# Kernel optimization log

Hardware: AMD Instinct MI355X
Metric: run time of the kernel (lower is better)

The kernel has to match this reference:

```python
import jax, jax.numpy as jnp
import numpy as np

D_MODEL = 512
N_HEADS = 8
D_FF = 2048
EPS = 1e-5


def _layernorm(x, g, b):
    mu = jnp.mean(x, axis=-1, keepdims=True)
    var = jnp.mean(jnp.square(x - mu), axis=-1, keepdims=True)
    return (x - mu) * jax.lax.rsqrt(var + EPS) * g + b


def setup_inputs() -> dict:
    key = jax.random.key(0)
    ks = jax.random.split(key, 12)
    B, N, C = 2, 2048, D_MODEL
    s = lambda fi, fo: 1.0 / np.sqrt(fi)
    inp = {
        "x": jax.random.normal(ks[0], (B, N, C), jnp.float32),
        # weights stored as [in, out] (y = x @ W + b)
        "qkv_w": jax.random.normal(ks[1], (C, 3 * C), jnp.float32) * s(C, 3 * C),
        "qkv_b": jnp.zeros((3 * C,), jnp.float32),
        "out_w": jax.random.normal(ks[2], (C, C), jnp.float32) * s(C, C),
        "out_b": jnp.zeros((C,), jnp.float32),
        "ffn_w1": jax.random.normal(ks[3], (C, D_FF), jnp.float32) * s(C, D_FF),
        "ffn_b1": jnp.zeros((D_FF,), jnp.float32),
        "ffn_w2": jax.random.normal(ks[4], (D_FF, C), jnp.float32) * s(D_FF, C),
        "ffn_b2": jnp.zeros((C,), jnp.float32),
        "n1_g": jnp.ones((C,), jnp.float32),
        "n1_b": jnp.zeros((C,), jnp.float32),
        "n2_g": jnp.ones((C,), jnp.float32),
        "n2_b": jnp.zeros((C,), jnp.float32),
        "conv_w": jax.random.normal(ks[5], (C, C, 3), jnp.float32) * s(3 * C, C),  # [out, in, k]
        "conv_b": jnp.zeros((C,), jnp.float32),
        "cn_g": jnp.ones((C,), jnp.float32),
        "cn_b": jnp.zeros((C,), jnp.float32),
    }
    return inp


def _forward(x, qkv_w, qkv_b, out_w, out_b, ffn_w1, ffn_b1, ffn_w2, ffn_b2,
             n1_g, n1_b, n2_g, n2_b, conv_w, conv_b, cn_g, cn_b):
    B, N, C = x.shape
    H, dk = N_HEADS, C // N_HEADS
    scale = 1.0 / np.sqrt(dk)

    # --- ProbSparse self-attention ---
    qkv = (x @ qkv_w + qkv_b).reshape(B, N, 3, H, dk)
    q, k, v = (jnp.moveaxis(qkv, (2, 3), (0, 2))[i] for i in range(3))  # each [B,H,N,dk]
    scores = jnp.einsum("bhnd,bhmd->bhnm", q, k) * scale  # [B,H,N,N]
    M = jnp.max(scores, axis=-1) - jnp.mean(scores, axis=-1)  # [B,H,N]
    n_top = max(1, min(int(N * 0.25), N - 1))
    _, top_idx = jax.lax.top_k(M, n_top)  # [B,H,n_top]
    bidx = jnp.arange(B)[:, None, None]
    hidx = jnp.arange(H)[None, :, None]
    row_sel = jnp.zeros((B, H, N), bool).at[bidx, hidx, top_idx].set(True)
    # rows not selected are fully masked (-1e9) -> uniform softmax, as in the original
    attn = jax.nn.softmax(jnp.where(row_sel[..., None], scores, -1e9), axis=-1)
    out = jnp.einsum("bhnm,bhmd->bhnd", attn, v)
    out = out.transpose(0, 2, 1, 3).reshape(B, N, C)
    attn_out = out @ out_w + out_b

    x = _layernorm(x + attn_out, n1_g, n1_b)

    # --- FFN (exact GELU) ---
    h = jax.nn.gelu(x @ ffn_w1 + ffn_b1, approximate=False)
    ffn_out = h @ ffn_w2 + ffn_b2
    x = _layernorm(x + ffn_out, n2_g, n2_b)

    # --- distilling conv: circular conv1d(k=3,p=1) -> maxpool(k=3,s=2,p=1) -> ELU -> LN ---
    xc = x.transpose(0, 2, 1)  # [B,C,N]
    xc = jnp.concatenate([xc[..., -1:], xc, xc[..., :1]], axis=-1)  # circular pad 1
    xc = jax.lax.conv_general_dilated(
        xc, conv_w, window_strides=(1,), padding="VALID",
        dimension_numbers=("NCH", "OIH", "NCH")) + conv_b[None, :, None]
    # maxpool k=3 s=2 p=1 (pad with -inf)
    neg = jnp.finfo(xc.dtype).min
    xc = jax.lax.reduce_window(xc, neg, jax.lax.max,
                               window_dimensions=(1, 1, 3), window_strides=(1, 1, 2),
                               padding=((0, 0), (0, 0), (1, 1)))
    x = xc.transpose(0, 2, 1)  # [B, N', C]
    x = _layernorm(jax.nn.elu(x), cn_g, cn_b)
    return x


def reference(x, qkv_w, qkv_b, out_w, out_b, ffn_w1, ffn_b1, ffn_w2, ffn_b2,
              n1_g, n1_b, n2_g, n2_b, conv_w, conv_b, cn_g, cn_b):
    return _forward(x, qkv_w, qkv_b, out_w, out_b, ffn_w1, ffn_b1, ffn_w2, ffn_b2,
                    n1_g, n1_b, n2_g, n2_b, conv_w, conv_b, cn_g, cn_b)
```

## Files before the change

kernel.cpp:

```cpp
#include <hip/hip_runtime.h>
#include <math.h>

#define NB 2
#define NN 2048
#define NC 512
#define NH 8
#define DK 64
#define DFF 2048
#define NTOP 512
#define NPOOL 1024
#define KSPLIT 4

typedef unsigned short u16;
typedef __attribute__((ext_vector_type(8))) short frag8;
typedef __attribute__((ext_vector_type(8))) _Float16 h8;
typedef __attribute__((ext_vector_type(4))) float f32x4;

static __device__ __forceinline__ u16 f2b(float f) {
    union { float f; unsigned int u; } v; v.f = f;
    unsigned int r = (v.u + 0x7fffu + ((v.u >> 16) & 1u)) >> 16;
    return (u16)r;
}
static __device__ __forceinline__ float b2f(u16 v) {
    union { unsigned u; float f; } x; x.u = ((unsigned)v) << 16; return x.f;
}
static __device__ __forceinline__ u16 f2h_bits(float f) {
    union { _Float16 h; u16 u; } v; v.h = (_Float16)f; return v.u;
}
static __device__ __forceinline__ float h2f_bits(u16 u) {
    union { u16 u; _Float16 h; } v; v.u = u; return (float)v.h;
}

template<int MODE>
__global__ __launch_bounds__(256) void mfma_gemm(const u16* __restrict__ A, int lda,
    const u16* __restrict__ Bt, const float* __restrict__ bias,
    float* __restrict__ C, u16* __restrict__ Cb, int ldc, int K, int act)
{
    __shared__ u16 As[128][72];
    __shared__ u16 Bs[128][72];
    int tid = threadIdx.x;
    int m0 = blockIdx.x * 128, n0 = blockIdx.y * 128;
    int wave = tid >> 6, lane = tid & 63;
    int ln = lane & 15, quad = lane >> 4;
    int wm = (wave >> 1) * 64, wn = (wave & 1) * 64;
    f32x4 acc[4][4] = {};
    for (int k0 = 0; k0 < K; k0 += 64) {
        #pragma unroll
        for (int i = 0; i < 4; i++) {
            int t = tid + i * 256;
            int m = t >> 3, kq = t & 7;
            size_t aoff;
            if (MODE == 1) {
                int grow = m0 + m;
                int shift = (k0 >> 9) - 1;
                int arow = (grow & ~(NN - 1)) | ((grow + shift) & (NN - 1));
                aoff = (size_t)arow * NC + ((k0 & 511) + kq * 8);
            } else {
                aoff = (size_t)(m0 + m) * lda + k0 + kq * 8;
            }
            *(uint4*)&As[m][kq * 8] = *(const uint4*)&A[aoff];
            *(uint4*)&Bs[m][kq * 8] = *(const uint4*)&Bt[(size_t)(n0 + m) * K + k0 + kq * 8];
        }
        __syncthreads();
        #pragma unroll
        for (int kk = 0; kk < 2; kk++) {
            frag8 af[4], bf[4];
            #pragma unroll
            for (int i = 0; i < 4; i++) {
                af[i] = *(const frag8*)&As[wm + i * 16 + ln][kk * 32 + quad * 8];
                bf[i] = *(const frag8*)&Bs[wn + i * 16 + ln][kk * 32 + quad * 8];
            }
            #pragma unroll
            for (int i = 0; i < 4; i++)
                #pragma unroll
                for (int j = 0; j < 4; j++)
                    acc[i][j] = __builtin_amdgcn_mfma_f32_16x16x32_bf16(
                        af[i], bf[j], acc[i][j], 0, 0, 0);
        }
        __syncthreads();
    }
    #pragma unroll
    for (int i = 0; i < 4; i++) {
        #pragma unroll
        for (int j = 0; j < 4; j++) {
            int col = n0 + wn + j * 16 + ln;
            float bv = bias ? bias[col] : 0.f;
            #pragma unroll
            for (int r = 0; r < 4; r++) {
                int row = m0 + wm + i * 16 + quad * 4 + r;
                float v = acc[i][j][r] + bv;
                if (act == 1) v = 0.5f * v * (1.0f + erff(v * 0.70710678118654752f));
                if (Cb) Cb[(size_t)row * ldc + col] = f2b(v);
                else    C[(size_t)row * ldc + col] = v;
            }
        }
    }
}

template<int MODE>
__global__ __launch_bounds__(256) void mfma_gemm_sk(const u16* __restrict__ A, int lda,
    const u16* __restrict__ Bt, float* __restrict__ P0, float* __restrict__ P1,
    int ldc, int K)
{
    __shared__ u16 As[128][72];
    __shared__ u16 Bs[128][72];
    int tid = threadIdx.x;
    int m0 = blockIdx.x * 128, n0 = blockIdx.y * 128;
    int split = blockIdx.z;
    int K2 = K >> 1, kbeg = split * K2;
    int wave = tid >> 6, lane = tid & 63;
    int ln = lane & 15, quad = lane >> 4;
    int wm = (wave >> 1) * 64, wn = (wave & 1) * 64;
    f32x4 acc[4][4] = {};
    for (int k0 = kbeg; k0 < kbeg + K2; k0 += 64) {
        #pragma unroll
        for (int i = 0; i < 4; i++) {
            int t = tid + i * 256;
            int m = t >> 3, kq = t & 7;
            size_t aoff;
            if (MODE == 1) {
                int grow = m0 + m;
                int shift = (k0 >> 9) - 1;
                int arow = (grow & ~(NN - 1)) | ((grow + shift) & (NN - 1));
                aoff = (size_t)arow * NC + ((k0 & 511) + kq * 8);
            } else {
                aoff = (size_t)(m0 + m) * lda + k0 + kq * 8;
            }
            *(uint4*)&As[m][kq * 8] = *(const uint4*)&A[aoff];
            *(uint4*)&Bs[m][kq * 8] = *(const uint4*)&Bt[(size_t)(n0 + m) * K + k0 + kq * 8];
        }
        __syncthreads();
        #pragma unroll
        for (int kk = 0; kk < 2; kk++) {
            frag8 af[4], bf[4];
            #pragma unroll
            for (int i = 0; i < 4; i++) {
                af[i] = *(const frag8*)&As[wm + i * 16 + ln][kk * 32 + quad * 8];
                bf[i] = *(const frag8*)&Bs[wn + i * 16 + ln][kk * 32 + quad * 8];
            }
            #pragma unroll
            for (int i = 0; i < 4; i++)
                #pragma unroll
                for (int j = 0; j < 4; j++)
                    acc[i][j] = __builtin_amdgcn_mfma_f32_16x16x32_bf16(
                        af[i], bf[j], acc[i][j], 0, 0, 0);
        }
        __syncthreads();
    }
    float* P = split ? P1 : P0;
    #pragma unroll
    for (int i = 0; i < 4; i++) {
        #pragma unroll
        for (int j = 0; j < 4; j++) {
            int col = n0 + wn + j * 16 + ln;
            #pragma unroll
            for (int r = 0; r < 4; r++) {
                int row = m0 + wm + i * 16 + quad * 4 + r;
                P[(size_t)row * ldc + col] = acc[i][j][r];
            }
        }
    }
}

__global__ __launch_bounds__(256) void mfma_qkv(const u16* __restrict__ A,
    const u16* __restrict__ Bt, const float* __restrict__ bias,
    float* __restrict__ Qh, float* __restrict__ Kh, float* __restrict__ Vh,
    u16* __restrict__ Qcat, u16* __restrict__ Kcat)
{
    __shared__ u16 As[128][72];
    __shared__ u16 Bs[128][72];
    int tid = threadIdx.x;
    int m0 = blockIdx.x * 128, n0 = blockIdx.y * 128;
    int wave = tid >> 6, lane = tid & 63;
    int ln = lane & 15, quad = lane >> 4;
    int wm = (wave >> 1) * 64, wn = (wave & 1) * 64;
    f32x4 acc[4][4] = {};
    for (int k0 = 0; k0 < 1024; k0 += 64) {
        #pragma unroll
        for (int i = 0; i < 4; i++) {
            int t = tid + i * 256;
            int m = t >> 3, kq = t & 7;
            *(uint4*)&As[m][kq * 8] = *(const uint4*)&A[(size_t)(m0 + m) * 1024 + k0 + kq * 8];
            *(uint4*)&Bs[m][kq * 8] = *(const uint4*)&Bt[(size_t)(n0 + m) * 1024 + k0 + kq * 8];
        }
        __syncthreads();
        #pragma unroll
        for (int kk = 0; kk < 2; kk++) {
            h8 af[4], bf[4];
            #pragma unroll
            for (int i = 0; i < 4; i++) {
                af[i] = *(const h8*)&As[wm + i * 16 + ln][kk * 32 + quad * 8];
                bf[i] = *(const h8*)&Bs[wn + i * 16 + ln][kk * 32 + quad * 8];
            }
            #pragma unroll
            for (int i = 0; i < 4; i++)
                #pragma unroll
                for (int j = 0; j < 4; j++)
                    acc[i][j] = __builtin_amdgcn_mfma_f32_16x16x32_f16(
                        af[i], bf[j], acc[i][j], 0, 0, 0);
        }
        __syncthreads();
    }
    #pragma unroll
    for (int i = 0; i < 4; i++) {
        #pragma unroll
        for (int j = 0; j < 4; j++) {
            int col = n0 + wn + j * 16 + ln;
            float bv = bias[col];
            int which = col >> 9;
            int h = (col >> 6) & 7, d = col & 63;
            #pragma unroll
            for (int r = 0; r < 4; r++) {
                int row = m0 + wm + i * 16 + quad * 4 + r;
                int b = row >> 11, n = row & (NN - 1);
                float v = acc[i][j][r] + bv;
                size_t off32 = ((size_t)((b << 3) + h) * NN + n) * DK + d;
                if (which == 2) {
                    Vh[off32] = v;
                } else {
                    size_t offc = ((size_t)((b << 3) + h) * NN + n) * 128 + d;
                    u16 hb_ = f2h_bits(v);
                    u16 lb_ = f2h_bits(v - h2f_bits(hb_));
                    if (which == 0) {
                        Qh[off32] = v;
                        Qcat[offc] = hb_; Qcat[offc + 64] = lb_;
                    } else {
                        Kh[off32] = v;
                        Kcat[offc] = hb_; Kcat[offc + 64] = lb_;
                    }
                }
            }
        }
    }
}

__global__ __launch_bounds__(256) void castw_t(const float* __restrict__ in,
    u16* __restrict__ out, int R, int C, int ldi, int coff)
{
    __shared__ float t[32][33];
    int c0 = blockIdx.x * 32, r0 = blockIdx.y * 32;
    int lx = threadIdx.x & 31, ly = threadIdx.x >> 5;
    #pragma unroll
    for (int i = 0; i < 4; i++)
        t[ly + i * 8][lx] = in[(size_t)(r0 + ly + i * 8) * ldi + coff + c0 + lx];
    __syncthreads();
    #pragma unroll
    for (int i = 0; i < 4; i++)
        out[(size_t)(c0 + ly + i * 8) * R + r0 + lx] = f2b(t[lx][ly + i * 8]);
}

__global__ __launch_bounds__(256) void castw_hl(const float* __restrict__ in,
    u16* __restrict__ out)
{
    __shared__ float t[32][33];
    int c0 = blockIdx.x * 32, r0 = blockIdx.y * 32;
    int lx = threadIdx.x & 31, ly = threadIdx.x >> 5;
    #pragma unroll
    for (int i = 0; i < 4; i++)
        t[ly + i * 8][lx] = in[(size_t)(r0 + ly + i * 8) * 1536 + c0 + lx];
    __syncthreads();
    #pragma unroll
    for (int i = 0; i < 4; i++) {
        float v = t[lx][ly + i * 8];
        u16 hb_ = f2h_bits(v);
        u16 lb_ = f2h_bits(v - h2f_bits(hb_));
        size_t ob = (size_t)(c0 + ly + i * 8) * 1024 + r0 + lx;
        out[ob] = hb_;
        out[ob + 512] = lb_;
    }
}

__global__ void castconvw_k(const float* __restrict__ cw, u16* __restrict__ out)
{
    int i = blockIdx.x * 256 + threadIdx.x;
    if (i >= 3 * NC * NC) return;
    int t = i % 3, ci = (i / 3) & (NC - 1), co = i / (3 * NC);
    out[(size_t)co * 1536 + t * NC + ci] = f2b(cw[i]);
}

__global__ void castx_k(const float* __restrict__ in, u16* __restrict__ xcat)
{
    int i = blockIdx.x * 256 + threadIdx.x;
    if (i >= (NB * NN * NC) / 4) return;
    int m = i >> 7, kq = i & 127;
    float4 v = ((const float4*)in)[i];
    ushort4 h, l;
    h.x = f2h_bits(v.x); h.y = f2h_bits(v.y);
    h.z = f2h_bits(v.z); h.w = f2h_bits(v.w);
    l.x = f2h_bits(v.x - h2f_bits(h.x));
    l.y = f2h_bits(v.y - h2f_bits(h.y));
    l.z = f2h_bits(v.z - h2f_bits(h.z));
    l.w = f2h_bits(v.w - h2f_bits(h.w));
    *(ushort4*)&xcat[(size_t)m * 1024 + kq * 4] = h;
    *(ushort4*)&xcat[(size_t)m * 1024 + 512 + kq * 4] = l;
}

__global__ __launch_bounds__(256) void castkv_k(const float* __restrict__ Kh,
    const float* __restrict__ Vh, u16* __restrict__ Kb, u16* __restrict__ Vtb)
{
    int bh = blockIdx.y;
    int n0 = blockIdx.x * 64;
    __shared__ float vt[64][68];
    int tid = threadIdx.x;
    const float* kin = Kh + ((size_t)bh * NN + n0) * DK;
    u16* kout = Kb + ((size_t)bh * NN + n0) * DK;
    const float* vin = Vh + ((size_t)bh * NN + n0) * DK;
    #pragma unroll
    for (int i = 0; i < 4; i++) {
        int t = tid + i * 256;
        int n = t >> 4, dq = t & 15;
        float4 v = *(const float4*)&kin[(size_t)n * DK + dq * 4];
        ushort4 o;
        o.x = f2b(v.x); o.y = f2b(v.y); o.z = f2b(v.z); o.w = f2b(v.w);
        *(ushort4*)&kout[(size_t)n * DK + dq * 4] = o;
        float4 w = *(const float4*)&vin[(size_t)n * DK + dq * 4];
        vt[dq * 4 + 0][n] = w.x; vt[dq * 4 + 1][n] = w.y;
        vt[dq * 4 + 2][n] = w.z; vt[dq * 4 + 3][n] = w.w;
    }
    __syncthreads();
    #pragma unroll
    for (int i = 0; i < 4; i++) {
        int t = tid + i * 256;
        int d = t >> 4, nq = t & 15;
        float4 v = *(const float4*)&vt[d][nq * 4];
        ushort4 o;
        o.x = f2b(v.x); o.y = f2b(v.y); o.z = f2b(v.z); o.w = f2b(v.w);
        *(ushort4*)&Vtb[((size_t)bh * DK + d) * NN + n0 + nq * 4] = o;
    }
}

__global__ __launch_bounds__(256) void meanv_part_k(const float* __restrict__ Vh,
    float* __restrict__ pmean)
{
    int bh = blockIdx.y, chunk = blockIdx.x;
    int tid = threadIdx.x;
    int d = tid & 63, sub = tid >> 6;
    const float* vb = Vh + ((size_t)bh * NN + chunk * 64 + sub * 16) * DK;
    float s = 0.f;
    #pragma unroll
    for (int r = 0; r < 16; r++) s += vb[(size_t)r * DK + d];
    __shared__ float red[256];
    red[tid] = s;
    __syncthreads();
    if (sub == 0)
        pmean[((size_t)bh * 32 + chunk) * 64 + d] =
            red[d] + red[64 + d] + red[128 + d] + red[192 + d];
}

__global__ void meanv_comb_k(const float* __restrict__ pmean, float* __restrict__ meanv)
{
    int bh = blockIdx.x;
    int d = threadIdx.x;
    float s = 0.f;
    #pragma unroll
    for (int c = 0; c < 32; c++) s += pmean[((size_t)bh * 32 + c) * 64 + d];
    meanv[bh * DK + d] = s * (1.0f / (float)NN);
}

__global__ __launch_bounds__(256) void rowstat_mfma_k(const u16* __restrict__ Qcat,
    const u16* __restrict__ Kcat, float* __restrict__ Marr, float* __restrict__ rowmax)
{
    int bh = blockIdx.x;
    int m0 = blockIdx.y * 64;
    int tid = threadIdx.x;
    int wave = tid >> 6, lane = tid & 63;
    int ln = lane & 15, quad = lane >> 4;
    __shared__ u16 Ks[128][136];
    h8 qf[4];
    {
        const u16* qp = &Qcat[((size_t)bh * NN + m0 + wave * 16 + ln) * 128];
        #pragma unroll
        for (int ks = 0; ks < 4; ks++)
            qf[ks] = *(const h8*)&qp[ks * 32 + quad * 8];
    }
    f32x4 vmax, vsum;
    #pragma unroll
    for (int r = 0; r < 4; r++) { vmax[r] = -INFINITY; vsum[r] = 0.f; }
    const u16* kB = Kcat + (size_t)bh * NN * 128;
    for (int nc = 0; nc < NN; nc += 128) {
        __syncthreads();
        #pragma unroll
        for (int i = 0; i < 8; i++) {
            int e = tid + i * 256;
            int n = e >> 4, kq = e & 15;
            *(uint4*)&Ks[n][kq * 8] = *(const uint4*)&kB[(size_t)(nc + n) * 128 + kq * 8];
        }
        __syncthreads();
        f32x4 accS[8] = {};
        #pragma unroll
        for (int nt = 0; nt < 8; nt++) {
            #pragma unroll
            for (int ks = 0; ks < 4; ks++) {
                h8 kf = *(const h8*)&Ks[nt * 16 + ln][ks * 32 + quad * 8];
                accS[nt] = __builtin_amdgcn_mfma_f32_16x16x32_f16(
                    qf[ks], kf, accS[nt], 0, 0, 0);
            }
        }
        #pragma unroll
        for (int nt = 0; nt < 8; nt++)
            #pragma unroll
            for (int r = 0; r < 4; r++) {
                vmax[r] = fmaxf(vmax[r], accS[nt][r]);
                vsum[r] += accS[nt][r];
            }
    }
    #pragma unroll
    for (int r = 0; r < 4; r++) {
        float mx = vmax[r], sm = vsum[r];
        #pragma unroll
        for (int off = 1; off < 16; off <<= 1) {
            mx = fmaxf(mx, __shfl_xor(mx, off));
            sm += __shfl_xor(sm, off);
        }
        if (ln == 0) {
            int m = m0 + wave * 16 + quad * 4 + r;
            Marr[(size_t)bh * NN + m] = (mx - sm * (1.0f / (float)NN)) * 0.125f;
            rowmax[(size_t)bh * NN + m] = mx * 0.125f;
        }
    }
}

__global__ __launch_bounds__(256) void topk_k(const float* __restrict__ Marr,
                                              int* __restrict__ idx)
{
    int bh = blockIdx.x;
    const float* Mr = Marr + (size_t)bh * NN;
    int* idxr = idx + (size_t)bh * NTOP;
    __shared__ int hist[256];
    __shared__ int suf[256];
    __shared__ int wred[4], wred2[4];
    __shared__ int bin_sh, rank_sh;
    int tid = threadIdx.x;
    int lane = tid & 63, w = tid >> 6;
    unsigned prefix = 0;
    int rank = NTOP;
    for (int pass = 0; pass < 4; pass++) {
        int shift = 24 - pass * 8;
        unsigned mask_hi = (pass == 0) ? 0u : (0xFFFFFFFFu << (shift + 8));
        hist[tid] = 0;
        __syncthreads();
        for (int i = tid; i < NN; i += 256) {
            union { float f; unsigned u; } v; v.f = Mr[i];
            unsigned k = (v.u & 0x80000000u) ? ~v.u : (v.u | 0x80000000u);
            if ((k & mask_hi) == prefix)
                atomicAdd(&hist[(k >> shift) & 255], 1);
        }
        __syncthreads();
        int v = hist[tid];
        #pragma unroll
        for (int off = 1; off < 64; off <<= 1) {
            int t = __shfl_down(v, off);
            if (lane + off < 64) v += t;
        }
        if (lane == 0) wred[w] = v;
        __syncthreads();
        int add = 0;
        #pragma unroll
        for (int w2 = 0; w2 < 4; w2++) if (w2 > w) add += wred[w2];
        suf[tid] = v + add;
        __syncthreads();
        int sv = suf[tid];
        int nxt = (tid < 255) ? suf[tid + 1] : 0;
        if (sv >= rank && nxt < rank) { bin_sh = tid; rank_sh = rank - nxt; }
        __syncthreads();
        prefix |= ((unsigned)bin_sh << shift);
        rank = rank_sh;
        __syncthreads();
    }
    union { unsigned u; float f; } tv;
    tv.u = (prefix & 0x80000000u) ? (prefix & 0x7FFFFFFFu) : ~prefix;
    float thr = tv.f;
    int lg = 0, le = 0;
    #pragma unroll
    for (int k = 0; k < 8; k++) {
        float v = Mr[tid * 8 + k];
        lg += (v > thr) ? 1 : 0;
        le += (v == thr) ? 1 : 0;
    }
    int vg = lg, ve = le;
    #pragma unroll
    for (int off = 1; off < 64; off <<= 1) {
        int tg = __shfl_up(vg, off);
        int te = __shfl_up(ve, off);
        if (lane >= off) { vg += tg; ve += te; }
    }
    if (lane == 63) { wred[w] = vg; wred2[w] = ve; }
    __syncthreads();
    int addg = 0, adde = 0, totg = 0;
    #pragma unroll
    for (int w2 = 0; w2 < 4; w2++) {
        totg += wred[w2];
        if (w2 < w) { addg += wred[w2]; adde += wred2[w2]; }
    }
    int cnt_gt = totg;
    int needed = NTOP - cnt_gt;
    int gpre = (vg + addg) - lg, epre = (ve + adde) - le;
    #pragma unroll
    for (int k = 0; k < 8; k++) {
        int p = tid * 8 + k;
        float v = Mr[p];
        bool isgt = v > thr, iseq = v == thr;
        bool selv = isgt || (iseq && epre < needed);
        if (selv) idxr[gpre + (epre < needed ? epre : needed)] = p;
        gpre += isgt ? 1 : 0;
        epre += iseq ? 1 : 0;
    }
}

__global__ void fill_k(const float* __restrict__ meanv, u16* __restrict__ ctxb)
{
    int i = blockIdx.x * 256 + threadIdx.x;
    if (i >= NB * NN * NC) return;
    int c = i & (NC - 1);
    int m = i >> 9;
    int b = m >> 11;
    int h = c >> 6, d = c & 63;
    ctxb[i] = f2b(meanv[(((b << 3) + h) << 6) + d]);
}

__global__ __launch_bounds__(256) void attn_mfma_k(const float* __restrict__ Qh,
    const u16* __restrict__ Kb, const u16* __restrict__ Vtb,
    const int* __restrict__ idx, const float* __restrict__ rowmax,
    float* __restrict__ Opart, float* __restrict__ ml)
{
    int yy = blockIdx.x;
    int bh = yy >> 2, split = yy & (KSPLIT - 1);
    int t0 = blockIdx.y * 64;
    int tid = threadIdx.x;
    int wave = tid >> 6, lane = tid & 63;
    int ln = lane & 15, quad = lane >> 4;
    __shared__ u16 Ks[128][72];
    __shared__ u16 Vt[64][136];
    __shared__ u16 Ps[4][16][136];
    __shared__ int rows[64];
    if (tid < 64) rows[tid] = idx[bh * NTOP + t0 + tid];
    __syncthreads();
    frag8 qf[2];
    {
        const float* qp = &Qh[((size_t)bh * NN + rows[wave * 16 + ln]) * DK];
        #pragma unroll
        for (int ks = 0; ks < 2; ks++) {
            float4 a = *(const float4*)&qp[ks * 32 + quad * 8];
            float4 b = *(const float4*)&qp[ks * 32 + quad * 8 + 4];
            union { frag8 f; u16 s[8]; } u;
            u.s[0] = f2b(a.x * 0.125f); u.s[1] = f2b(a.y * 0.125f);
            u.s[2] = f2b(a.z * 0.125f); u.s[3] = f2b(a.w * 0.125f);
            u.s[4] = f2b(b.x * 0.125f); u.s[5] = f2b(b.y * 0.125f);
            u.s[6] = f2b(b.z * 0.125f); u.s[7] = f2b(b.w * 0.125f);
            qf[ks] = u.f;
        }
    }
    float rm[4];
    #pragma unroll
    for (int r = 0; r < 4; r++)
        rm[r] = rowmax[(size_t)bh * NN + rows[wave * 16 + quad * 4 + r]];
    f32x4 accO[4] = {};
    float lrun[4] = {};
    const u16* kbB = Kb + (size_t)bh * NN * DK;
    const u16* vtB = Vtb + (size_t)bh * DK * NN;
    int nc0 = split * (NN / KSPLIT);
    for (int nc = nc0; nc < nc0 + NN / KSPLIT; nc += 128) {
        __syncthreads();
        #pragma unroll
        for (int i = 0; i < 4; i++) {
            int e = tid + i * 256;
            int n = e >> 3, kq = e & 7;
            *(uint4*)&Ks[n][kq * 8] = *(const uint4*)&kbB[(size_t)(nc + n) * DK + kq * 8];
        }
        #pragma unroll
        for (int i = 0; i < 4; i++) {
            int e = tid + i * 256;
            int d = e >> 4, nq = e & 15;
            *(uint4*)&Vt[d][nq * 8] = *(const uint4*)&vtB[(size_t)d * NN + nc + nq * 8];
        }
        __syncthreads();
        f32x4 accS[8] = {};
        #pragma unroll
        for (int nt = 0; nt < 8; nt++) {
            frag8 b0 = *(const frag8*)&Ks[nt * 16 + ln][quad * 8];
            frag8 b1 = *(const frag8*)&Ks[nt * 16 + ln][32 + quad * 8];
            accS[nt] = __builtin_amdgcn_mfma_f32_16x16x32_bf16(qf[0], b0, accS[nt], 0, 0, 0);
            accS[nt] = __builtin_amdgcn_mfma_f32_16x16x32_bf16(qf[1], b1, accS[nt], 0, 0, 0);
        }
        #pragma unroll
        for (int nt = 0; nt < 8; nt++)
            #pragma unroll
            for (int r = 0; r < 4; r++) {
                float p = expf(accS[nt][r] - rm[r]);
                accS[nt][r] = p;
                lrun[r] += p;
            }
        #pragma unroll
        for (int nt = 0; nt < 8; nt++)
            #pragma unroll
            for (int r = 0; r < 4; r++)
                Ps[wave][quad * 4 + r][nt * 16 + ln] = f2b(accS[nt][r]);
        #pragma unroll
        for (int ks = 0; ks < 4; ks++) {
            frag8 pf = *(const frag8*)&Ps[wave][ln][ks * 32 + quad * 8];
            #pragma unroll
            for (int nt2 = 0; nt2 < 4; nt2++) {
                frag8 vf = *(const frag8*)&Vt[nt2 * 16 + ln][ks * 32 + quad * 8];
                accO[nt2] = __builtin_amdgcn_mfma_f32_16x16x32_bf16(pf, vf, accO[nt2], 0, 0, 0);
            }
        }
    }
    #pragma unroll
    for (int r = 0; r < 4; r++) {
        float ls = lrun[r];
        #pragma unroll
        for (int off = 1; off < 16; off <<= 1) ls += __shfl_xor(ls, off);
        int p = t0 + wave * 16 + quad * 4 + r;
        size_t pb = ((size_t)bh * NTOP + p) * KSPLIT + split;
        #pragma unroll
        for (int nt2 = 0; nt2 < 4; nt2++)
            Opart[pb * 64 + nt2 * 16 + ln] = accO[nt2][r];
        if (ln == 0) ml[pb * 2 + 1] = ls;
    }
}

__global__ __launch_bounds__(256) void attn_comb_k(const float* __restrict__ Opart,
    const float* __restrict__ ml, const int* __restrict__ idx,
    u16* __restrict__ ctxb)
{
    int gid = blockIdx.x * 4 + (threadIdx.x >> 6);
    int lane = threadIdx.x & 63;
    int bh = gid >> 9;
    int h = bh & 7, b = bh >> 3;
    size_t base = (size_t)gid * KSPLIT;
    float L = 0.f, O = 0.f;
    #pragma unroll
    for (int s = 0; s < KSPLIT; s++) {
        L += ml[(base + s) * 2 + 1];
        O += Opart[(base + s) * 64 + lane];
    }
    int n = idx[gid];
    ctxb[((size_t)(b * NN + n)) * NC + h * DK + lane] = f2b(O / L);
}

__global__ __launch_bounds__(256) void ln_k(const float* __restrict__ A,
    const float* __restrict__ P0, const float* __restrict__ P1,
    const float* __restrict__ cb,
    const float* __restrict__ g, const float* __restrict__ bb,
    float* __restrict__ out, u16* __restrict__ outb)
{
    int row = blockIdx.x;
    int tid = threadIdx.x;
    __shared__ float v[NC];
    __shared__ float red[256];
    size_t base = (size_t)row * NC;
    for (int i = tid; i < NC; i += 256)
        v[i] = A[base + i] + P0[base + i] + P1[base + i] + cb[i];
    __syncthreads();
    float ls = 0.f;
    for (int i = tid; i < NC; i += 256) ls += v[i];
    red[tid] = ls; __syncthreads();
    for (int off = 128; off > 0; off >>= 1) {
        if (tid < off) red[tid] += red[tid + off];
        __syncthreads();
    }
    float mu = red[0] / (float)NC;
    __syncthreads();
    float lv = 0.f;
    for (int i = tid; i < NC; i += 256) { float d = v[i] - mu; lv += d * d; }
    red[tid] = lv; __syncthreads();
    for (int off = 128; off > 0; off >>= 1) {
        if (tid < off) red[tid] += red[tid + off];
        __syncthreads();
    }
    float rstd = rsqrtf(red[0] / (float)NC + 1e-5f);
    for (int i = tid; i < NC; i += 256) {
        float r = (v[i] - mu) * rstd * g[i] + bb[i];
        if (out) out[base + i] = r;
        if (outb) outb[base + i] = f2b(r);
    }
}

__global__ __launch_bounds__(256) void pool_ln_k(const float* __restrict__ P0,
    const float* __restrict__ P1, const float* __restrict__ cb,
    const float* __restrict__ g, const float* __restrict__ bb,
    float* __restrict__ outp)
{
    int row = blockIdx.x;
    int j = row & (NPOOL - 1), b = row / NPOOL;
    int tid = threadIdx.x;
    __shared__ float v[NC];
    __shared__ float red[256];
    size_t bbase = (size_t)b * NN * NC;
    for (int i = tid; i < NC; i += 256) {
        float m = -INFINITY;
        int p0 = 2 * j - 1;
        float cbv = cb[i];
        #pragma unroll
        for (int t = 0; t < 3; t++) {
            int p = p0 + t;
            if (p >= 0 && p < NN) {
                size_t off = bbase + (size_t)p * NC + i;
                m = fmaxf(m, P0[off] + P1[off] + cbv);
            }
        }
        v[i] = m > 0.f ? m : expm1f(m);
    }
    __syncthreads();
    float ls = 0.f;
    for (int i = tid; i < NC; i += 256) ls += v[i];
    red[tid] = ls; __syncthreads();
    for (int off = 128; off > 0; off >>= 1) {
        if (tid < off) red[tid] += red[tid + off];
        __syncthreads();
    }
    float mu = red[0] / (float)NC;
    __syncthreads();
    float lv = 0.f;
    for (int i = tid; i < NC; i += 256) { float d = v[i] - mu; lv += d * d; }
    red[tid] = lv; __syncthreads();
    for (int off = 128; off > 0; off >>= 1) {
        if (tid < off) red[tid] += red[tid + off];
        __syncthreads();
    }
    float rstd = rsqrtf(red[0] / (float)NC + 1e-5f);
    for (int i = tid; i < NC; i += 256)
        outp[(size_t)row * NC + i] = (v[i] - mu) * rstd * g[i] + bb[i];
}

extern "C" void kernel_launch(void* const* d_in, const int* in_sizes, int n_in,
                              void* d_out, int out_size, void* d_ws, size_t ws_size,
                              hipStream_t stream)
{
    (void)in_sizes; (void)n_in; (void)out_size; (void)ws_size;
    const float* x      = (const float*)d_in[0];
    const float* qkv_w  = (const float*)d_in[1];
    const float* qkv_b  = (const float*)d_in[2];
    const float* out_w  = (const float*)d_in[3];
    const float* out_b  = (const float*)d_in[4];
    const float* ffn_w1 = (const float*)d_in[5];
    const float* ffn_b1 = (const float*)d_in[6];
    const float* ffn_w2 = (const float*)d_in[7];
    const float* ffn_b2 = (const float*)d_in[8];
    const float* n1_g   = (const float*)d_in[9];
    const float* n1_b   = (const float*)d_in[10];
    const float* n2_g   = (const float*)d_in[11];
    const float* n2_b   = (const float*)d_in[12];
    const float* conv_w = (const float*)d_in[13];
    const float* conv_b = (const float*)d_in[14];
    const float* cn_g   = (const float*)d_in[15];
    const float* cn_b   = (const float*)d_in[16];

    const size_t R = (size_t)NB * NN * NC;
    float* ws = (float*)d_ws;
    float* x1   = ws;
    float* reg2 = ws + R;
    float* Qh   = ws + 2 * R;
    float* Kh   = ws + 3 * R;
    float* Vh   = ws + 4 * R;
    size_t o = 5 * R;
    float* pmax  = ws + o;  o += 65536;
    float* psum  = ws + o;  o += 65536;
    float* Marr  = ws + o;  o += 32768;
    float* pmean = ws + o;  o += 32768;
    float* meanv = ws + o;  o += 1024;
    int*   idx   = (int*)(ws + o);  o += 8192;
    float* ml    = ws + o;  o += 65536;
    u16*   ctxb  = (u16*)(ws + o);  o += R / 2;
    u16*   x1b   = (u16*)(ws + o);  o += R / 2;
    u16*   x2b   = (u16*)(ws + o);  o += R / 2;
    u16*   owT   = (u16*)(ws + o);  o += 131072;
    u16*   w1T   = (u16*)(ws + o);  o += 524288;
    u16*   w2T   = (u16*)(ws + o);  o += 524288;
    u16*   cwT   = (u16*)(ws + o);  o += 393216;
    u16*   Kb    = (u16*)reg2;
    u16*   Vtb   = (u16*)(ws + R + R / 2);
    float* Opart    = x1;
    u16*   hb       = (u16*)(ws + 3 * R);
    float* rowmax   = pmax;
    float* skP0 = reg2;
    float* skP1 = Vh;
    u16*   xcat  = (u16*)reg2;
    u16*   wcatT = w1T;
    u16*   Qcat  = x1b;
    u16*   Kcat  = (u16*)x1;
    (void)psum;

    castw_t<<<dim3(16, 16), 256, 0, stream>>>(out_w, owT, 512, 512, 512, 0);
    castconvw_k<<<3072, 256, 0, stream>>>(conv_w, cwT);
    castx_k<<<2048, 256, 0, stream>>>(x, xcat);
    castw_hl<<<dim3(48, 16), 256, 0, stream>>>(qkv_w, wcatT);

    mfma_qkv<<<dim3(32, 12), 256, 0, stream>>>(xcat, wcatT, qkv_b,
                                               Qh, Kh, Vh, Qcat, Kcat);

    castw_t<<<dim3(64, 16), 256, 0, stream>>>(ffn_w1, w1T, 512, 2048, 2048, 0);
    castw_t<<<dim3(16, 64), 256, 0, stream>>>(ffn_w2, w2T, 2048, 512, 512, 0);

    castkv_k<<<dim3(NN / 64, NB * NH), 256, 0, stream>>>(Kh, Vh, Kb, Vtb);

    meanv_part_k<<<dim3(32, NB * NH), 256, 0, stream>>>(Vh, pmean);
    meanv_comb_k<<<NB * NH, 64, 0, stream>>>(pmean, meanv);

    rowstat_mfma_k<<<dim3(NB * NH, NN / 64), 256, 0, stream>>>(Qcat, Kcat, Marr, rowmax);
    topk_k<<<NB * NH, 256, 0, stream>>>(Marr, idx);
    fill_k<<<((int)R + 255) / 256, 256, 0, stream>>>(meanv, ctxb);
    attn_mfma_k<<<dim3(NB * NH * KSPLIT, NTOP / 64), 256, 0, stream>>>(
        Qh, Kb, Vtb, idx, rowmax, Opart, ml);
    attn_comb_k<<<NB * NH * NTOP / 4, 256, 0, stream>>>(Opart, ml, idx, ctxb);

    mfma_gemm_sk<0><<<dim3(32, 4, 2), 256, 0, stream>>>(
        ctxb, NC, owT, skP0, skP1, NC, NC);

    ln_k<<<NB * NN, 256, 0, stream>>>(x, skP0, skP1, out_b, n1_g, n1_b, x1, x1b);

    mfma_gemm<0><<<dim3(32, 16), 256, 0, stream>>>(
        x1b, NC, w1T, ffn_b1, (float*)nullptr, hb, DFF, NC, 1);
    mfma_gemm_sk<0><<<dim3(32, 4, 2), 256, 0, stream>>>(
        hb, DFF, w2T, skP0, skP1, NC, DFF);

    ln_k<<<NB * NN, 256, 0, stream>>>(x1, skP0, skP1, ffn_b2,
                                      n2_g, n2_b, (float*)nullptr, x2b);

    mfma_gemm_sk<1><<<dim3(32, 4, 2), 256, 0, stream>>>(
        x2b, NC, cwT, skP0, skP1, NC, 1536);

    pool_ln_k<<<NB * NPOOL, 256, 0, stream>>>(skP0, skP1, conv_b, cn_g, cn_b,
                                              (float*)d_out);
}
```

Before: 332.1 us.

## Emit bf16 Q/K directly from QKV GEMM, fuse V cast with mean, vectorize fill

The QKV GEMM epilogue now writes pre-scaled bf16 Q and bf16 K directly instead of fp32 Q/K. This removes the separate K cast pass and the per-row fp32-to-bf16 conversion of Q in the attention kernel. The V transpose-cast kernel also computes the per-chunk partial V means from shared memory, which removes the separate mean kernel's global reread. fill_k writes 8 bf16 values per thread with vector loads and stores. The QKV epilogue still does scattered 2-byte stores, and the workspace aliasing was changed.

After: 324.2 us. -2.4%, faster.

```diff
diff --git a/kernel.cpp b/kernel.cpp
--- a/kernel.cpp
+++ b/kernel.cpp
@@ -164,7 +164,7 @@
 
 __global__ __launch_bounds__(256) void mfma_qkv(const u16* __restrict__ A,
     const u16* __restrict__ Bt, const float* __restrict__ bias,
-    float* __restrict__ Qh, float* __restrict__ Kh, float* __restrict__ Vh,
+    u16* __restrict__ Qbs, u16* __restrict__ Kb, float* __restrict__ Vh,
     u16* __restrict__ Qcat, u16* __restrict__ Kcat)
 {
     __shared__ u16 As[128][72];
@@ -222,10 +222,10 @@
                     u16 hb_ = f2h_bits(v);
                     u16 lb_ = f2h_bits(v - h2f_bits(hb_));
                     if (which == 0) {
-                        Qh[off32] = v;
+                        Qbs[off32] = f2b(v * 0.125f);
                         Qcat[offc] = hb_; Qcat[offc + 64] = lb_;
                     } else {
-                        Kh[off32] = v;
+                        Kb[off32] = f2b(v);
                         Kcat[offc] = hb_; Kcat[offc + 64] = lb_;
                     }
                 }
@@ -295,24 +295,19 @@
     *(ushort4*)&xcat[(size_t)m * 1024 + 512 + kq * 4] = l;
 }
 
-__global__ __launch_bounds__(256) void castkv_k(const float* __restrict__ Kh,
-    const float* __restrict__ Vh, u16* __restrict__ Kb, u16* __restrict__ Vtb)
+__global__ __launch_bounds__(256) void castv_k(const float* __restrict__ Vh,
+    u16* __restrict__ Vtb, float* __restrict__ pmean)
 {
     int bh = blockIdx.y;
     int n0 = blockIdx.x * 64;
     __shared__ float vt[64][68];
+    __shared__ float red[256];
     int tid = threadIdx.x;
-    const float* kin = Kh + ((size_t)bh * NN + n0) * DK;
-    u16* kout = Kb + ((size_t)bh * NN + n0) * DK;
     const float* vin = Vh + ((size_t)bh * NN + n0) * DK;
     #pragma unroll
     for (int i = 0; i < 4; i++) {
         int t = tid + i * 256;
         int n = t >> 4, dq = t & 15;
-        float4 v = *(const float4*)&kin[(size_t)n * DK + dq * 4];
-        ushort4 o;
-        o.x = f2b(v.x); o.y = f2b(v.y); o.z = f2b(v.z); o.w = f2b(v.w);
-        *(ushort4*)&kout[(size_t)n * DK + dq * 4] = o;
         float4 w = *(const float4*)&vin[(size_t)n * DK + dq * 4];
         vt[dq * 4 + 0][n] = w.x; vt[dq * 4 + 1][n] = w.y;
         vt[dq * 4 + 2][n] = w.z; vt[dq * 4 + 3][n] = w.w;
@@ -327,23 +322,14 @@
         o.x = f2b(v.x); o.y = f2b(v.y); o.z = f2b(v.z); o.w = f2b(v.w);
         *(ushort4*)&Vtb[((size_t)bh * DK + d) * NN + n0 + nq * 4] = o;
     }
-}
-
-__global__ __launch_bounds__(256) void meanv_part_k(const float* __restrict__ Vh,
-    float* __restrict__ pmean)
-{
-    int bh = blockIdx.y, chunk = blockIdx.x;
-    int tid = threadIdx.x;
     int d = tid & 63, sub = tid >> 6;
-    const float* vb = Vh + ((size_t)bh * NN + chunk * 64 + sub * 16) * DK;
     float s = 0.f;
     #pragma unroll
-    for (int r = 0; r < 16; r++) s += vb[(size_t)r * DK + d];
-    __shared__ float red[256];
+    for (int r = 0; r < 16; r++) s += vt[d][sub * 16 + r];
     red[tid] = s;
     __syncthreads();
     if (sub == 0)
-        pmean[((size_t)bh * 32 + chunk) * 64 + d] =
+        pmean[((size_t)bh * 32 + (n0 >> 6)) * 64 + d] =
             red[d] + red[64 + d] + red[128 + d] + red[192 + d];
 }
 
@@ -510,15 +496,21 @@
 __global__ void fill_k(const float* __restrict__ meanv, u16* __restrict__ ctxb)
 {
     int i = blockIdx.x * 256 + threadIdx.x;
-    if (i >= NB * NN * NC) return;
-    int c = i & (NC - 1);
-    int m = i >> 9;
+    if (i >= (NB * NN * NC) / 8) return;
+    int c = (i * 8) & (NC - 1);
+    int m = (i * 8) >> 9;
     int b = m >> 11;
     int h = c >> 6, d = c & 63;
-    ctxb[i] = f2b(meanv[(((b << 3) + h) << 6) + d]);
-}
-
-__global__ __launch_bounds__(256) void attn_mfma_k(const float* __restrict__ Qh,
+    const float* mv = &meanv[(((b << 3) + h) << 6) + d];
+    float4 v0 = *(const float4*)mv;
+    float4 v1 = *(const float4*)(mv + 4);
+    union { u16 s[8]; uint4 u; } r;
+    r.s[0] = f2b(v0.x); r.s[1] = f2b(v0.y); r.s[2] = f2b(v0.z); r.s[3] = f2b(v0.w);
+    r.s[4] = f2b(v1.x); r.s[5] = f2b(v1.y); r.s[6] = f2b(v1.z); r.s[7] = f2b(v1.w);
+    *(uint4*)&ctxb[(size_t)i * 8] = r.u;
+}
+
+__global__ __launch_bounds__(256) void attn_mfma_k(const u16* __restrict__ Qbs,
     const u16* __restrict__ Kb, const u16* __restrict__ Vtb,
     const int* __restrict__ idx, const float* __restrict__ rowmax,
     float* __restrict__ Opart, float* __restrict__ ml)
@@ -537,18 +529,9 @@
     __syncthreads();
     frag8 qf[2];
     {
-        const float* qp = &Qh[((size_t)bh * NN + rows[wave * 16 + ln]) * DK];
-        #pragma unroll
-        for (int ks = 0; ks < 2; ks++) {
-            float4 a = *(const float4*)&qp[ks * 32 + quad * 8];
-            float4 b = *(const float4*)&qp[ks * 32 + quad * 8 + 4];
-            union { frag8 f; u16 s[8]; } u;
-            u.s[0] = f2b(a.x * 0.125f); u.s[1] = f2b(a.y * 0.125f);
-            u.s[2] = f2b(a.z * 0.125f); u.s[3] = f2b(a.w * 0.125f);
-            u.s[4] = f2b(b.x * 0.125f); u.s[5] = f2b(b.y * 0.125f);
-            u.s[6] = f2b(b.z * 0.125f); u.s[7] = f2b(b.w * 0.125f);
-            qf[ks] = u.f;
-        }
+        const u16* qp = &Qbs[((size_t)bh * NN + rows[wave * 16 + ln]) * DK];
+        qf[0] = *(const frag8*)&qp[quad * 8];
+        qf[1] = *(const frag8*)&qp[32 + quad * 8];
     }
     float rm[4];
     #pragma unroll
@@ -750,7 +733,7 @@
     float* ws = (float*)d_ws;
     float* x1   = ws;
     float* reg2 = ws + R;
-    float* Qh   = ws + 2 * R;
+    float* QhR  = ws + 2 * R;
     float* Kh   = ws + 3 * R;
     float* Vh   = ws + 4 * R;
     size_t o = 5 * R;
@@ -768,10 +751,11 @@
     u16*   w1T   = (u16*)(ws + o);  o += 524288;
     u16*   w2T   = (u16*)(ws + o);  o += 524288;
     u16*   cwT   = (u16*)(ws + o);  o += 393216;
-    u16*   Kb    = (u16*)reg2;
+    u16*   Qbs   = (u16*)QhR;
+    u16*   Kb    = (u16*)(QhR + R / 2);
     u16*   Vtb   = (u16*)(ws + R + R / 2);
     float* Opart    = x1;
-    u16*   hb       = (u16*)(ws + 3 * R);
+    u16*   hb       = (u16*)Kh;
     float* rowmax   = pmax;
     float* skP0 = reg2;
     float* skP1 = Vh;
@@ -787,21 +771,19 @@
     castw_hl<<<dim3(48, 16), 256, 0, stream>>>(qkv_w, wcatT);
 
     mfma_qkv<<<dim3(32, 12), 256, 0, stream>>>(xcat, wcatT, qkv_b,
-                                               Qh, Kh, Vh, Qcat, Kcat);
+                                               Qbs, Kb, Vh, Qcat, Kcat);
 
     castw_t<<<dim3(64, 16), 256, 0, stream>>>(ffn_w1, w1T, 512, 2048, 2048, 0);
     castw_t<<<dim3(16, 64), 256, 0, stream>>>(ffn_w2, w2T, 2048, 512, 512, 0);
 
-    castkv_k<<<dim3(NN / 64, NB * NH), 256, 0, stream>>>(Kh, Vh, Kb, Vtb);
-
-    meanv_part_k<<<dim3(32, NB * NH), 256, 0, stream>>>(Vh, pmean);
+    castv_k<<<dim3(NN / 64, NB * NH), 256, 0, stream>>>(Vh, Vtb, pmean);
     meanv_comb_k<<<NB * NH, 64, 0, stream>>>(pmean, meanv);
 
     rowstat_mfma_k<<<dim3(NB * NH, NN / 64), 256, 0, stream>>>(Qcat, Kcat, Marr, rowmax);
     topk_k<<<NB * NH, 256, 0, stream>>>(Marr, idx);
-    fill_k<<<((int)R + 255) / 256, 256, 0, stream>>>(meanv, ctxb);
+    fill_k<<<(int)(R / 8 / 256), 256, 0, stream>>>(meanv, ctxb);
     attn_mfma_k<<<dim3(NB * NH * KSPLIT, NTOP / 64), 256, 0, stream>>>(
-        Qh, Kb, Vtb, idx, rowmax, Opart, ml);
+        Qbs, Kb, Vtb, idx, rowmax, Opart, ml);
     attn_comb_k<<<NB * NH * NTOP / 4, 256, 0, stream>>>(Opart, ml, idx, ctxb);
 
     mfma_gemm_sk<0><<<dim3(32, 4, 2), 256, 0, stream>>>(
```
